# Kernel optimization log

Measured on AMD Instinct MI355X. Metric: run time of the kernel, lower is better.

The kernel has to match this reference:

```python
import jax, jax.numpy as jnp
import numpy as np


def _forward(agent_qs, ally_states, enemy_states, W_al, b_al, W_en, b_en, Wq, bq, Wk, bk,
             w1_W1, w1_b1, w1_W2, w1_b2, wf_W1, wf_b1, wf_W2, wf_b2, hb_W, hb_b,
             v_W1, v_b1, v_W2, v_b2):
    A, B, S, _ = ally_states.shape
    E = A + enemy_states.shape[0]
    D = W_al.shape[1]
    Da = Wq.shape[1]
    # entity encoders: [A,B,S,D], [En,B,S,D]
    ally_embed = ally_states @ W_al + b_al
    enemy_embed = enemy_states @ W_en + b_en
    entity = jnp.concatenate([ally_embed, enemy_embed], axis=0)      # [E,B,S,D]
    ent_bs = jnp.transpose(entity, (1, 2, 0, 3))                     # [B,S,E,D]
    q = ent_bs @ Wq + bq                                             # [B,S,E,Da]
    k = ent_bs @ Wk + bk                                             # [B,S,E,Da]
    scale = jnp.asarray(Da, q.dtype) ** 0.5
    energy = jnp.einsum('bsid,bsjd->bsij', q / scale, k)             # [B,S,E,E]
    # torch softmax(dim=1) on [BS,E,E] == softmax over the query axis i
    attn = jax.nn.softmax(energy, axis=2)
    # bmm(value[BS,D,E], attn).mean(-1) == value @ mean_j attn[:, :, e, j]
    attn_mean = jnp.mean(attn, axis=3)                               # [B,S,E]
    attn_out = jnp.einsum('bsed,bse->bsd', ent_bs, attn_mean)        # [B,S,D]
    ally_bs = jnp.transpose(ally_embed, (1, 2, 0, 3))                # [B,S,A,D]
    emi = jnp.concatenate(
        [jnp.broadcast_to(attn_out[:, :, None, :], (B, S, A, D)), ally_bs], axis=-1)  # [B,S,A,2D]
    # hypernets (2-layer)
    w1 = jnp.abs(jax.nn.relu(emi @ w1_W1 + w1_b1) @ w1_W2 + w1_b2)   # [B,S,A,M]
    b1 = attn_out @ hb_W + hb_b                                      # [B,S,M]
    hidden = jax.nn.elu(jnp.einsum('bsa,bsam->bsm', agent_qs, w1) + b1)
    wf = jnp.abs(jax.nn.relu(attn_out @ wf_W1 + wf_b1) @ wf_W2 + wf_b2)  # [B,S,M]
    v = jax.nn.relu(attn_out @ v_W1 + v_b1) @ v_W2 + v_b2            # [B,S,1]
    q_tot = jnp.einsum('bsm,bsm->bs', hidden, wf)[..., None] + v     # [B,S,1]
    return q_tot


def setup_inputs() -> dict:
    key = jax.random.key(0)
    B, S, A, En = 128, 128, 8, 8
    NFal, NFen, D, Da, M, H = 32, 16, 64, 128, 32, 64
    ks = jax.random.split(key, 32)
    p = lambda i, shape: jax.random.normal(ks[i], shape, dtype=jnp.float32) * 0.05
    return dict(
        agent_qs=jax.random.normal(ks[0], (B, S, A), dtype=jnp.float32),
        ally_states=jax.random.normal(ks[1], (A, B, S, NFal), dtype=jnp.float32),
        enemy_states=jax.random.normal(ks[2], (En, B, S, NFen), dtype=jnp.float32),
        W_al=p(3, (NFal, D)), b_al=p(4, (D,)), W_en=p(5, (NFen, D)), b_en=p(6, (D,)),
        Wq=p(7, (D, Da)), bq=p(8, (Da,)), Wk=p(9, (D, Da)), bk=p(10, (Da,)),
        w1_W1=p(11, (2 * D, H)), w1_b1=p(12, (H,)), w1_W2=p(13, (H, M)), w1_b2=p(14, (M,)),
        wf_W1=p(15, (D, H)), wf_b1=p(16, (H,)), wf_W2=p(17, (H, M)), wf_b2=p(18, (M,)),
        hb_W=p(19, (D, M)), hb_b=p(20, (M,)),
        v_W1=p(21, (D, M)), v_b1=p(22, (M,)), v_W2=p(23, (M, 1)), v_b2=p(24, (1,)),
    )


def reference(agent_qs, ally_states, enemy_states, W_al, b_al, W_en, b_en, Wq, bq, Wk, bk,
              w1_W1, w1_b1, w1_W2, w1_b2, wf_W1, wf_b1, wf_W2, wf_b2, hb_W, hb_b,
              v_W1, v_b1, v_W2, v_b2):
    return _forward(agent_qs, ally_states, enemy_states, W_al, b_al, W_en, b_en, Wq, bq, Wk, bk,
                    w1_W1, w1_b1, w1_W2, w1_b2, wf_W1, wf_b1, wf_W2, wf_b2, hb_W, hb_b,
                    v_W1, v_b1, v_W2, v_b2)
```

## Files before the change

kernel.cpp:

```cpp
#include <hip/hip_runtime.h>
#include <hip/hip_bf16.h>


#define B_   128
#define S_   128
#define BS_  (B_ * S_)
#define INV_S 0.08838834764831845f

typedef short bs8 __attribute__((ext_vector_type(8)));
typedef float f4  __attribute__((ext_vector_type(4)));

#define MFMA(a, b, c) __builtin_amdgcn_mfma_f32_16x16x32_bf16((a), (b), (c), 0, 0, 0)
#define LOADB(t) (*(const bs8*)&fb[(size_t)(t) * 512 + lane * 8])

__device__ __forceinline__ short f2bf(float f) {
    union { float f; unsigned u; } v; v.f = f;
    unsigned r = v.u + 0x7fffu + ((v.u >> 16) & 1u);
    return (short)(r >> 16);
}

__global__ __launch_bounds__(64)
void qmix_pre1(const float* __restrict__ Wq, const float* __restrict__ Wk,
               const float* __restrict__ bk,
               float* __restrict__ Ms, float* __restrict__ vq)
{
    const int blk = blockIdx.x, t = threadIdx.x;
    float p;
    if (blk < 4096) {
        const int k = blk >> 6, n = blk & 63;
        p = Wq[k * 128 + t] * Wk[n * 128 + t]
          + Wq[k * 128 + 64 + t] * Wk[n * 128 + 64 + t];
        #pragma unroll
        for (int off = 32; off >= 1; off >>= 1) p += __shfl_down(p, off, 64);
        if (t == 0) Ms[k * 64 + n] = p * INV_S;
    } else {
        const int d = blk - 4096;
        p = Wq[d * 128 + t] * bk[t] + Wq[d * 128 + 64 + t] * bk[64 + t];
        #pragma unroll
        for (int off = 32; off >= 1; off >>= 1) p += __shfl_down(p, off, 64);
        if (t == 0) vq[d] = p * INV_S;
    }
}

__global__ __launch_bounds__(64)
void qmix_pack(const float* __restrict__ Ms,
               const float* __restrict__ W_al, const float* __restrict__ W_en,
               const float* __restrict__ w1_W1, const float* __restrict__ w1_W2,
               const float* __restrict__ vq,
               short* __restrict__ fb)
{
    const int blk = blockIdx.x, lane = threadIdx.x;
    const int quad = lane >> 4, l16 = lane & 15;
    bs8 v;
    if (blk < 8) {
        const int ks = blk >> 2, n = (blk & 3) * 16 + l16;
        #pragma unroll
        for (int j = 0; j < 8; ++j)
            v[j] = f2bf(Ms[(ks * 32 + quad * 8 + j) * 64 + n]);
    } else if (blk < 16) {
        const bool en = (blk >= 12);
        const float* W = en ? W_en : W_al;
        const int Krows = en ? 16 : 32;
        const int n = ((blk - (en ? 12 : 8)) & 3) * 16 + l16;
        #pragma unroll
        for (int j = 0; j < 8; ++j) {
            const int k = quad * 8 + j;
            v[j] = (k < Krows) ? f2bf(W[k * 64 + n]) : (short)0;
        }
    } else if (blk < 32) {
        const int t = blk - 16, ks = t >> 2, n = (t & 3) * 16 + l16;
        #pragma unroll
        for (int j = 0; j < 8; ++j)
            v[j] = f2bf(w1_W1[(ks * 32 + quad * 8 + j) * 64 + n]);
    } else if (blk < 36) {
        const int t = blk - 32, ks = t >> 1, n = (t & 1) * 16 + l16;
        #pragma unroll
        for (int j = 0; j < 8; ++j)
            v[j] = f2bf(w1_W2[(ks * 32 + quad * 8 + j) * 32 + n]);
    } else {
        const int ks = blk - 36;
        #pragma unroll
        for (int j = 0; j < 8; ++j)
            v[j] = (l16 == 0) ? f2bf(vq[ks * 32 + quad * 8 + j]) : (short)0;
    }
    *(bs8*)&fb[(size_t)blk * 512 + lane * 8] = v;
}

__global__ __launch_bounds__(64)
void qmix_main(const float* __restrict__ agent_qs,
               const float* __restrict__ ally, const float* __restrict__ enemy,
               const float* __restrict__ b_al, const float* __restrict__ b_en,
               const float* __restrict__ w1_b1, const float* __restrict__ w1_b2,
               const float* __restrict__ wf_W1, const float* __restrict__ wf_b1,
               const float* __restrict__ wf_W2, const float* __restrict__ wf_b2,
               const float* __restrict__ hb_W,  const float* __restrict__ hb_b,
               const float* __restrict__ v_W1,  const float* __restrict__ v_b1,
               const float* __restrict__ v_W2,  const float* __restrict__ v_b2,
               const short* __restrict__ fb,
               float* __restrict__ out)
{
    const int site = blockIdx.x;
    const int lane = threadIdx.x, quad = lane >> 4, l16 = lane & 15;

    __shared__ __align__(16) short s_entb[16][72];
    __shared__ __align__(16) short s_scr[16][72];
    __shared__ __align__(16) float s_aoutf[64];
    __shared__ __align__(16) short s_aoutb[64];
    __shared__ __align__(16) float s_h[64];
    __shared__ __align__(16) float s_red[4][32];
    __shared__ float s_b1[32], s_hv[32], s_qs[8];

    if (lane < 8) s_qs[lane] = agent_qs[(size_t)site * 8 + lane];

    bs8 a_al = {0,0,0,0,0,0,0,0}, a_en = {0,0,0,0,0,0,0,0};
    if (l16 < 8) {
        const float* pa = ally + ((size_t)l16 * BS_ + site) * 32 + quad * 8;
        const float4 f0 = *(const float4*)pa, f1 = *(const float4*)(pa + 4);
        a_al[0]=f2bf(f0.x); a_al[1]=f2bf(f0.y); a_al[2]=f2bf(f0.z); a_al[3]=f2bf(f0.w);
        a_al[4]=f2bf(f1.x); a_al[5]=f2bf(f1.y); a_al[6]=f2bf(f1.z); a_al[7]=f2bf(f1.w);
    } else if (quad < 2) {
        const float* pe = enemy + ((size_t)(l16 - 8) * BS_ + site) * 16 + quad * 8;
        const float4 f0 = *(const float4*)pe, f1 = *(const float4*)(pe + 4);
        a_en[0]=f2bf(f0.x); a_en[1]=f2bf(f0.y); a_en[2]=f2bf(f0.z); a_en[3]=f2bf(f0.w);
        a_en[4]=f2bf(f1.x); a_en[5]=f2bf(f1.y); a_en[6]=f2bf(f1.z); a_en[7]=f2bf(f1.w);
    }

    f4 encf[4];
    #pragma unroll
    for (int n0t = 0; n0t < 4; ++n0t) {
        f4 acc = {0.f, 0.f, 0.f, 0.f};
        acc = MFMA(a_al, LOADB(8 + n0t), acc);
        acc = MFMA(a_en, LOADB(12 + n0t), acc);
        const int d = n0t * 16 + l16;
        const float bal = b_al[d], ben = b_en[d];
        #pragma unroll
        for (int r = 0; r < 4; ++r) {
            const int row = quad * 4 + r;
            const float v = acc[r] + (row < 8 ? bal : ben);
            encf[n0t][r] = v;
            s_entb[row][d] = f2bf(v);
        }
    }
    __syncthreads();

    const bs8 ae0 = *(const bs8*)&s_entb[l16][quad * 8];
    const bs8 ae1 = *(const bs8*)&s_entb[l16][32 + quad * 8];
    f4 pqacc = {0.f, 0.f, 0.f, 0.f};
    pqacc = MFMA(ae0, LOADB(36), pqacc);
    pqacc = MFMA(ae1, LOADB(37), pqacc);
    #pragma unroll
    for (int n0t = 0; n0t < 4; ++n0t) {
        f4 acc = {0.f, 0.f, 0.f, 0.f};
        acc = MFMA(ae0, LOADB(0 + n0t), acc);
        acc = MFMA(ae1, LOADB(4 + n0t), acc);
        const int d = n0t * 16 + l16;
        #pragma unroll
        for (int r = 0; r < 4; ++r) s_scr[quad * 4 + r][d] = f2bf(acc[r]);
    }
    __syncthreads();

    f4 eacc = {0.f, 0.f, 0.f, 0.f};
    {
        const bs8 at0 = *(const bs8*)&s_scr[l16][quad * 8];
        const bs8 at1 = *(const bs8*)&s_scr[l16][32 + quad * 8];
        eacc = MFMA(at0, ae0, eacc);
        eacc = MFMA(at1, ae1, eacc);
        const int src = lane & 48;
        #pragma unroll
        for (int r = 0; r < 4; ++r) eacc[r] += __shfl(pqacc[r], src, 64);
    }

    float amean_r[4];
    {
        float cmax = fmaxf(fmaxf(eacc[0], eacc[1]), fmaxf(eacc[2], eacc[3]));
        cmax = fmaxf(cmax, __shfl_xor(cmax, 16, 64));
        cmax = fmaxf(cmax, __shfl_xor(cmax, 32, 64));
        float er[4], csum = 0.f;
        #pragma unroll
        for (int r = 0; r < 4; ++r) { er[r] = __expf(eacc[r] - cmax); csum += er[r]; }
        csum += __shfl_xor(csum, 16, 64);
        csum += __shfl_xor(csum, 32, 64);
        const float inv = 1.f / csum;
        #pragma unroll
        for (int r = 0; r < 4; ++r) {
            float p = er[r] * inv;
            p += __shfl_xor(p, 1, 64);
            p += __shfl_xor(p, 2, 64);
            p += __shfl_xor(p, 4, 64);
            p += __shfl_xor(p, 8, 64);
            amean_r[r] = p * (1.f / 16.f);
        }
    }

    #pragma unroll
    for (int n0t = 0; n0t < 4; ++n0t) {
        float ap = amean_r[0] * encf[n0t][0] + amean_r[1] * encf[n0t][1]
                 + amean_r[2] * encf[n0t][2] + amean_r[3] * encf[n0t][3];
        ap += __shfl_xor(ap, 16, 64);
        ap += __shfl_xor(ap, 32, 64);
        if (quad == 0) {
            s_aoutf[n0t * 16 + l16] = ap;
            s_aoutb[n0t * 16 + l16] = f2bf(ap);
        }
    }
    __syncthreads();

    {
        const float* Wx = (lane < 32) ? (hb_W + lane) : (v_W1 + (lane - 32));
        float acc_wf = wf_b1[lane];
        float acc_x  = (lane < 32) ? hb_b[lane] : v_b1[lane - 32];
        #pragma unroll 4
        for (int d4 = 0; d4 < 16; ++d4) {
            const int r = d4 * 4;
            const float4 av = *(const float4*)&s_aoutf[r];
            acc_wf += av.x * wf_W1[(r + 0) * 64 + lane] + av.y * wf_W1[(r + 1) * 64 + lane]
                    + av.z * wf_W1[(r + 2) * 64 + lane] + av.w * wf_W1[(r + 3) * 64 + lane];
            acc_x  += av.x * Wx[(r + 0) * 32] + av.y * Wx[(r + 1) * 32]
                    + av.z * Wx[(r + 2) * 32] + av.w * Wx[(r + 3) * 32];
        }
        s_h[lane] = fmaxf(acc_wf, 0.f);
        if (lane < 32) s_b1[lane] = acc_x;
        else           s_hv[lane - 32] = fmaxf(acc_x, 0.f) * v_W2[lane - 32];
    }
    __syncthreads();

    float wfm = 0.f;
    if (lane < 32) {
        float a2 = wf_b2[lane];
        #pragma unroll 4
        for (int t4 = 0; t4 < 16; ++t4) {
            const int r = t4 * 4;
            const float4 h4 = *(const float4*)&s_h[r];
            a2 += h4.x * wf_W2[(r + 0) * 32 + lane] + h4.y * wf_W2[(r + 1) * 32 + lane]
                + h4.z * wf_W2[(r + 2) * 32 + lane] + h4.w * wf_W2[(r + 3) * 32 + lane];
        }
        wfm = fabsf(a2);
    }

    {
        const bs8 a0 = *(const bs8*)&s_aoutb[quad * 8];
        const bs8 a1 = *(const bs8*)&s_aoutb[32 + quad * 8];
        f4 hacc[4];
        #pragma unroll
        for (int n0t = 0; n0t < 4; ++n0t) {
            f4 acc = {0.f, 0.f, 0.f, 0.f};
            acc = MFMA(a0,  LOADB(16 + 0 + n0t), acc);
            acc = MFMA(a1,  LOADB(16 + 4 + n0t), acc);
            acc = MFMA(ae0, LOADB(16 + 8 + n0t), acc);
            acc = MFMA(ae1, LOADB(16 + 12 + n0t), acc);
            hacc[n0t] = acc;
        }
        #pragma unroll
        for (int n0t = 0; n0t < 4; ++n0t) {
            const int d = n0t * 16 + l16;
            const float b1v = w1_b1[d];
            #pragma unroll
            for (int r = 0; r < 4; ++r) {
                const int row = quad * 4 + r;
                if (row < 8)
                    s_scr[row][d] = f2bf(fmaxf(hacc[n0t][r] + b1v, 0.f));
            }
        }
    }
    __syncthreads();

    {
        const bs8 ah0 = *(const bs8*)&s_scr[l16][quad * 8];
        const bs8 ah1 = *(const bs8*)&s_scr[l16][32 + quad * 8];
        #pragma unroll
        for (int n0t = 0; n0t < 2; ++n0t) {
            f4 acc = {0.f, 0.f, 0.f, 0.f};
            acc = MFMA(ah0, LOADB(32 + 0 + n0t), acc);
            acc = MFMA(ah1, LOADB(32 + 2 + n0t), acc);
            const int col = n0t * 16 + l16;
            const float b2v = w1_b2[col];
            float p = 0.f;
            if (quad < 2) {
                #pragma unroll
                for (int r = 0; r < 4; ++r)
                    p += s_qs[quad * 4 + r] * fabsf(acc[r] + b2v);
            }
            s_red[quad][col] = p;
        }
    }
    __syncthreads();

    float contrib = 0.f;
    if (lane < 32) {
        float hp = s_red[0][lane] + s_red[1][lane] + s_red[2][lane] + s_red[3][lane]
                 + s_b1[lane];
        hp = (hp > 0.f) ? hp : (__expf(hp) - 1.f);
        contrib = hp * wfm + s_hv[lane];
    }
    #pragma unroll
    for (int off = 16; off >= 1; off >>= 1)
        contrib += __shfl_down(contrib, off, 64);
    if (lane == 0) out[site] = contrib + v_b2[0];
}

extern "C" void kernel_launch(void* const* d_in, const int* in_sizes, int n_in,
                              void* d_out, int out_size, void* d_ws, size_t ws_size,
                              hipStream_t stream) {
    const float* p[25];
    for (int i = 0; i < 25; ++i) p[i] = (const float*)d_in[i];
    short* fb = (short*)d_ws;
    float* vq = (float*)((char*)d_ws + 38 * 512 * 2);
    float* Ms = vq + 64;

    qmix_pre1<<<4096 + 64, 64, 0, stream>>>(p[7], p[9], p[10], Ms, vq);
    qmix_pack<<<38, 64, 0, stream>>>(Ms, p[3], p[5], p[11], p[13], vq, fb);
    qmix_main<<<BS_, 64, 0, stream>>>(
        p[0], p[1], p[2], p[4], p[6], p[12], p[14],
        p[15], p[16], p[17], p[18], p[19], p[20], p[21], p[22], p[23], p[24],
        fb, (float*)d_out);
}
```

Baseline: 174.9 us.

## Pack two site-waves per block and replace LDS reductions with shuffles

The main kernel now runs two independent sites per block. Each of the two waves gets its own LDS struct, and the grid is halved. The final per-column reduction (s_red), the b1 values and the v-hidden values now travel between lanes through cross-lane shuffles instead of shared memory, which removes one barrier and some LDS traffic. The aim is to ease per-block launch and scheduling limits on how many waves a CU can hold with 64-thread blocks. The trade-off is that each barrier now couples two unrelated waves.

```diff
diff --git a/kernel.cpp b/kernel.cpp
--- a/kernel.cpp
+++ b/kernel.cpp
@@ -5,6 +5,7 @@
 #define B_   128
 #define S_   128
 #define BS_  (B_ * S_)
+#define WPB  2
 #define INV_S 0.08838834764831845f
 
 typedef short bs8 __attribute__((ext_vector_type(8)));
@@ -86,7 +87,16 @@
     *(bs8*)&fb[(size_t)blk * 512 + lane * 8] = v;
 }
 
-__global__ __launch_bounds__(64)
+struct __align__(16) WaveLds {
+    short entb[16][72];
+    short scr[16][72];
+    float aoutf[64];
+    short aoutb[64];
+    float h[64];
+    float qs[8];
+};
+
+__global__ __launch_bounds__(64 * WPB)
 void qmix_main(const float* __restrict__ agent_qs,
                const float* __restrict__ ally, const float* __restrict__ enemy,
                const float* __restrict__ b_al, const float* __restrict__ b_en,
@@ -99,18 +109,15 @@
                const short* __restrict__ fb,
                float* __restrict__ out)
 {
-    const int site = blockIdx.x;
-    const int lane = threadIdx.x, quad = lane >> 4, l16 = lane & 15;
-
-    __shared__ __align__(16) short s_entb[16][72];
-    __shared__ __align__(16) short s_scr[16][72];
-    __shared__ __align__(16) float s_aoutf[64];
-    __shared__ __align__(16) short s_aoutb[64];
-    __shared__ __align__(16) float s_h[64];
-    __shared__ __align__(16) float s_red[4][32];
-    __shared__ float s_b1[32], s_hv[32], s_qs[8];
-
-    if (lane < 8) s_qs[lane] = agent_qs[(size_t)site * 8 + lane];
+    const int w    = threadIdx.x >> 6;
+    const int lane = threadIdx.x & 63;
+    const int site = blockIdx.x * WPB + w;
+    const int quad = lane >> 4, l16 = lane & 15;
+
+    __shared__ WaveLds lds[WPB];
+    WaveLds& L = lds[w];
+
+    if (lane < 8) L.qs[lane] = agent_qs[(size_t)site * 8 + lane];
 
     bs8 a_al = {0,0,0,0,0,0,0,0}, a_en = {0,0,0,0,0,0,0,0};
     if (l16 < 8) {
@@ -138,13 +145,13 @@
             const int row = quad * 4 + r;
             const float v = acc[r] + (row < 8 ? bal : ben);
             encf[n0t][r] = v;
-            s_entb[row][d] = f2bf(v);
-        }
-    }
-    __syncthreads();
-
-    const bs8 ae0 = *(const bs8*)&s_entb[l16][quad * 8];
-    const bs8 ae1 = *(const bs8*)&s_entb[l16][32 + quad * 8];
+            L.entb[row][d] = f2bf(v);
+        }
+    }
+    __syncthreads();
+
+    const bs8 ae0 = *(const bs8*)&L.entb[l16][quad * 8];
+    const bs8 ae1 = *(const bs8*)&L.entb[l16][32 + quad * 8];
     f4 pqacc = {0.f, 0.f, 0.f, 0.f};
     pqacc = MFMA(ae0, LOADB(36), pqacc);
     pqacc = MFMA(ae1, LOADB(37), pqacc);
@@ -155,14 +162,14 @@
         acc = MFMA(ae1, LOADB(4 + n0t), acc);
         const int d = n0t * 16 + l16;
         #pragma unroll
-        for (int r = 0; r < 4; ++r) s_scr[quad * 4 + r][d] = f2bf(acc[r]);
+        for (int r = 0; r < 4; ++r) L.scr[quad * 4 + r][d] = f2bf(acc[r]);
     }
     __syncthreads();
 
     f4 eacc = {0.f, 0.f, 0.f, 0.f};
     {
-        const bs8 at0 = *(const bs8*)&s_scr[l16][quad * 8];
-        const bs8 at1 = *(const bs8*)&s_scr[l16][32 + quad * 8];
+        const bs8 at0 = *(const bs8*)&L.scr[l16][quad * 8];
+        const bs8 at1 = *(const bs8*)&L.scr[l16][32 + quad * 8];
         eacc = MFMA(at0, ae0, eacc);
         eacc = MFMA(at1, ae1, eacc);
         const int src = lane & 48;
@@ -199,12 +206,13 @@
         ap += __shfl_xor(ap, 16, 64);
         ap += __shfl_xor(ap, 32, 64);
         if (quad == 0) {
-            s_aoutf[n0t * 16 + l16] = ap;
-            s_aoutb[n0t * 16 + l16] = f2bf(ap);
-        }
-    }
-    __syncthreads();
-
+            L.aoutf[n0t * 16 + l16] = ap;
+            L.aoutb[n0t * 16 + l16] = f2bf(ap);
+        }
+    }
+    __syncthreads();
+
+    float b1m = 0.f, hvp = 0.f;
     {
         const float* Wx = (lane < 32) ? (hb_W + lane) : (v_W1 + (lane - 32));
         float acc_wf = wf_b1[lane];
@@ -212,16 +220,17 @@
         #pragma unroll 4
         for (int d4 = 0; d4 < 16; ++d4) {
             const int r = d4 * 4;
-            const float4 av = *(const float4*)&s_aoutf[r];
+            const float4 av = *(const float4*)&L.aoutf[r];
             acc_wf += av.x * wf_W1[(r + 0) * 64 + lane] + av.y * wf_W1[(r + 1) * 64 + lane]
                     + av.z * wf_W1[(r + 2) * 64 + lane] + av.w * wf_W1[(r + 3) * 64 + lane];
             acc_x  += av.x * Wx[(r + 0) * 32] + av.y * Wx[(r + 1) * 32]
                     + av.z * Wx[(r + 2) * 32] + av.w * Wx[(r + 3) * 32];
         }
-        s_h[lane] = fmaxf(acc_wf, 0.f);
-        if (lane < 32) s_b1[lane] = acc_x;
-        else           s_hv[lane - 32] = fmaxf(acc_x, 0.f) * v_W2[lane - 32];
-    }
+        L.h[lane] = fmaxf(acc_wf, 0.f);
+        if (lane < 32) b1m = acc_x;
+        else           hvp = fmaxf(acc_x, 0.f) * v_W2[lane - 32];
+    }
+    const float hvx = __shfl_xor(hvp, 32, 64);
     __syncthreads();
 
     float wfm = 0.f;
@@ -230,7 +239,7 @@
         #pragma unroll 4
         for (int t4 = 0; t4 < 16; ++t4) {
             const int r = t4 * 4;
-            const float4 h4 = *(const float4*)&s_h[r];
+            const float4 h4 = *(const float4*)&L.h[r];
             a2 += h4.x * wf_W2[(r + 0) * 32 + lane] + h4.y * wf_W2[(r + 1) * 32 + lane]
                 + h4.z * wf_W2[(r + 2) * 32 + lane] + h4.w * wf_W2[(r + 3) * 32 + lane];
         }
@@ -238,8 +247,8 @@
     }
 
     {
-        const bs8 a0 = *(const bs8*)&s_aoutb[quad * 8];
-        const bs8 a1 = *(const bs8*)&s_aoutb[32 + quad * 8];
+        const bs8 a0 = *(const bs8*)&L.aoutb[quad * 8];
+        const bs8 a1 = *(const bs8*)&L.aoutb[32 + quad * 8];
         f4 hacc[4];
         #pragma unroll
         for (int n0t = 0; n0t < 4; ++n0t) {
@@ -258,15 +267,16 @@
             for (int r = 0; r < 4; ++r) {
                 const int row = quad * 4 + r;
                 if (row < 8)
-                    s_scr[row][d] = f2bf(fmaxf(hacc[n0t][r] + b1v, 0.f));
+                    L.scr[row][d] = f2bf(fmaxf(hacc[n0t][r] + b1v, 0.f));
             }
         }
     }
     __syncthreads();
 
-    {
-        const bs8 ah0 = *(const bs8*)&s_scr[l16][quad * 8];
-        const bs8 ah1 = *(const bs8*)&s_scr[l16][32 + quad * 8];
+    float p0 = 0.f, p1 = 0.f;
+    {
+        const bs8 ah0 = *(const bs8*)&L.scr[l16][quad * 8];
+        const bs8 ah1 = *(const bs8*)&L.scr[l16][32 + quad * 8];
         #pragma unroll
         for (int n0t = 0; n0t < 2; ++n0t) {
             f4 acc = {0.f, 0.f, 0.f, 0.f};
@@ -278,19 +288,19 @@
             if (quad < 2) {
                 #pragma unroll
                 for (int r = 0; r < 4; ++r)
-                    p += s_qs[quad * 4 + r] * fabsf(acc[r] + b2v);
+                    p += L.qs[quad * 4 + r] * fabsf(acc[r] + b2v);
             }
-            s_red[quad][col] = p;
-        }
-    }
-    __syncthreads();
+            if (n0t == 0) p0 = p; else p1 = p;
+        }
+        p0 += __shfl_xor(p0, 16, 64);
+        p1 += __shfl_xor(p1, 16, 64);
+    }
 
     float contrib = 0.f;
     if (lane < 32) {
-        float hp = s_red[0][lane] + s_red[1][lane] + s_red[2][lane] + s_red[3][lane]
-                 + s_b1[lane];
+        float hp = (lane < 16 ? p0 : p1) + b1m;
         hp = (hp > 0.f) ? hp : (__expf(hp) - 1.f);
-        contrib = hp * wfm + s_hv[lane];
+        contrib = hp * wfm + hvx;
     }
     #pragma unroll
     for (int off = 16; off >= 1; off >>= 1)
@@ -309,7 +319,7 @@
 
     qmix_pre1<<<4096 + 64, 64, 0, stream>>>(p[7], p[9], p[10], Ms, vq);
     qmix_pack<<<38, 64, 0, stream>>>(Ms, p[3], p[5], p[11], p[13], vq, fb);
-    qmix_main<<<BS_, 64, 0, stream>>>(
+    qmix_main<<<BS_ / WPB, 64 * WPB, 0, stream>>>(
         p[0], p[1], p[2], p[4], p[6], p[12], p[14],
         p[15], p[16], p[17], p[18], p[19], p[20], p[21], p[22], p[23], p[24],
         fb, (float*)d_out);
```

Result: no change. 173.0 us (-1.1%).
